# Kernel optimization log

Hardware: AMD Instinct MI355X
Metric: run time of the kernel (lower is better)

Reference implementation:

```python
import jax, jax.numpy as jnp
import numpy as np

NEG_SLOPE = 0.2


def add_self_loops(edge_index, num_nodes):
    loop = jnp.arange(num_nodes, dtype=edge_index.dtype)
    src = jnp.concatenate([edge_index[0], loop])
    dst = jnp.concatenate([edge_index[1], loop])
    return src, dst


def gat_conv(x, src, dst, W, att_src, att_dst, bias, heads, out_ch, concat):
    N = x.shape[0]
    h = (x @ W).reshape(N, heads, out_ch)                      # [N,H,C]
    a_src = jnp.sum(h * att_src, axis=-1)                      # [N,H]
    a_dst = jnp.sum(h * att_dst, axis=-1)                      # [N,H]
    e = a_src[src] + a_dst[dst]                                # [E,H]
    e = jax.nn.leaky_relu(e, NEG_SLOPE)
    # segment softmax over incoming edges of each destination node
    m = jax.ops.segment_max(e, dst, num_segments=N)            # [N,H]
    m = jnp.where(jnp.isfinite(m), m, 0.0)
    ex = jnp.exp(e - m[dst])
    s = jax.ops.segment_sum(ex, dst, num_segments=N)           # [N,H]
    alpha = ex / jnp.where(s[dst] > 0, s[dst], 1.0)            # [E,H]
    msg = alpha[:, :, None] * h[src]                           # [E,H,C]
    out = jax.ops.segment_sum(msg, dst, num_segments=N)        # [N,H,C]
    if concat:
        out = out.reshape(N, heads * out_ch)
    else:
        out = out.mean(axis=1)
    return out + bias


def setup_inputs() -> dict:
    key = jax.random.key(0)
    ks = jax.random.split(key, 10)
    N, F, E, H, C1 = 50000, 128, 800000, 8, 8
    x = jax.random.normal(ks[0], (N, F), dtype=jnp.float32)
    edge_index = jax.random.randint(ks[1], (2, E), 0, N, dtype=jnp.int64)
    sc = 0.1
    W1 = jax.random.normal(ks[2], (F, H * C1), dtype=jnp.float32) * sc
    a_src1 = jax.random.normal(ks[3], (H, C1), dtype=jnp.float32) * sc
    a_dst1 = jax.random.normal(ks[4], (H, C1), dtype=jnp.float32) * sc
    b1 = jnp.zeros((H * C1,), dtype=jnp.float32)
    W2 = jax.random.normal(ks[5], (H * C1, F), dtype=jnp.float32) * sc
    a_src2 = jax.random.normal(ks[6], (1, F), dtype=jnp.float32) * sc
    a_dst2 = jax.random.normal(ks[7], (1, F), dtype=jnp.float32) * sc
    b2 = jnp.zeros((F,), dtype=jnp.float32)
    return {"x": x, "edge_index": edge_index, "W1": W1, "a_src1": a_src1,
            "a_dst1": a_dst1, "b1": b1, "W2": W2, "a_src2": a_src2,
            "a_dst2": a_dst2, "b2": b2}


def reference(x, edge_index, W1, a_src1, a_dst1, b1, W2, a_src2, a_dst2, b2):
    N = x.shape[0]
    src, dst = add_self_loops(edge_index, N)
    h = gat_conv(x, src, dst, W1, a_src1, a_dst1, b1, heads=8, out_ch=8, concat=True)
    h = jax.nn.elu(h)
    out = gat_conv(h, src, dst, W2, a_src2, a_dst2, b2, heads=1, out_ch=x.shape[1], concat=True)
    return out
```

## Files before the change

### kernel.cpp

```cpp
#include <hip/hip_runtime.h>
#include <hip/hip_fp16.h>
#include <math.h>

#define NEG_SLOPE 0.2f
#define BSTRIDE 6144

typedef _Float16 f16x8 __attribute__((ext_vector_type(8)));
typedef float    f32x4 __attribute__((ext_vector_type(4)));

__device__ __forceinline__ void get_edge(const int* __restrict__ ei, int E, int e,
                                         int& s, int& d) {
    if (e < E) { s = ei[e]; d = ei[E + e]; }
    else       { s = e - E; d = e - E; }
}

union G1SMem {
    unsigned int sWu[4096];
    struct {
        int lhist[256], lbase[256], lrank[256], gbase[256];
        unsigned int sbuf[4096];
        int saddr[4096];
    } sc;
};

__global__ __launch_bounds__(256) void g1s_kernel(const float* __restrict__ x,
                                                  const float* __restrict__ W,
                                                  const float* __restrict__ asrc,
                                                  const float* __restrict__ adst,
                                                  _Float16* __restrict__ hout,
                                                  float* __restrict__ av,
                                                  float* __restrict__ bv, int N,
                                                  int gblocks,
                                                  const float* __restrict__ W2,
                                                  const float* __restrict__ as2,
                                                  const float* __restrict__ ad2,
                                                  float* __restrict__ wa,
                                                  float* __restrict__ wb,
                                                  int* __restrict__ bcur,
                                                  const int* __restrict__ ei, int E, int ET,
                                                  unsigned int* __restrict__ bstore,
                                                  int nbuck) {
    __shared__ G1SMem sm;
    int t = threadIdx.x;

    if (blockIdx.x == (unsigned)gblocks) {
        if (t < 64) {
            const float* wr = W2 + t * 128;
            float sa = 0.f, sb = 0.f;
#pragma unroll 8
            for (int c = 0; c < 128; ++c) {
                float w = wr[c];
                sa = fmaf(w, as2[c], sa);
                sb = fmaf(w, ad2[c], sb);
            }
            wa[t] = sa; wb[t] = sb;
        }
        return;
    }

    if (blockIdx.x > (unsigned)gblocks) {
        int sblk = blockIdx.x - gblocks - 1;
        int start = sblk * 4096;
        int cnt = ET - start; if (cnt > 4096) cnt = 4096;
        sm.sc.lhist[t] = 0; sm.sc.lrank[t] = 0;
        __syncthreads();
        int mybuck[16]; unsigned int myval[16];
#pragma unroll
        for (int k = 0; k < 16; ++k) {
            int e = start + t + k * 256;
            mybuck[k] = -1;
            if (e < ET) {
                int s, d; get_edge(ei, E, e, s, d);
                mybuck[k] = d >> 8;
                myval[k] = ((unsigned int)d << 16) | (unsigned int)s;
                atomicAdd(&sm.sc.lhist[mybuck[k]], 1);
            }
        }
        __syncthreads();
        int v = sm.sc.lhist[t];
        sm.sc.lbase[t] = v;
        __syncthreads();
        for (int off = 1; off < 256; off <<= 1) {
            int u = (t >= off) ? sm.sc.lbase[t - off] : 0;
            __syncthreads();
            sm.sc.lbase[t] += u;
            __syncthreads();
        }
        int excl = sm.sc.lbase[t] - v;
        if (t < nbuck && v > 0)
            sm.sc.gbase[t] = t * BSTRIDE + atomicAdd(&bcur[t], v);
        __syncthreads();
        sm.sc.lbase[t] = excl;
        __syncthreads();
#pragma unroll
        for (int k = 0; k < 16; ++k) {
            int b = mybuck[k];
            if (b >= 0) {
                int r = atomicAdd(&sm.sc.lrank[b], 1);
                int idx = sm.sc.lbase[b] + r;
                sm.sc.sbuf[idx] = myval[k];
                sm.sc.saddr[idx] = sm.sc.gbase[b] + r;
            }
        }
        __syncthreads();
        for (int j = t; j < cnt; j += 256)
            bstore[sm.sc.saddr[j]] = sm.sc.sbuf[j];
        return;
    }

    for (int p = t; p < 4096; p += 256) {
        int frag = p >> 8;
        int lane = (p >> 2) & 63;
        int j2   = p & 3;
        int chunk = frag >> 2, nt = frag & 3;
        int k = chunk * 32 + ((lane >> 4) << 3) + (j2 << 1);
        int n = nt * 16 + (lane & 15);
        union { _Float16 h[2]; unsigned int u; } pk;
        pk.h[0] = (_Float16)W[k * 64 + n];
        pk.h[1] = (_Float16)W[(k + 1) * 64 + n];
        sm.sWu[p] = pk.u;
    }
    __syncthreads();

    int lane = t & 63;
    int wid  = t >> 6;
    int rbase = blockIdx.x * 64 + wid * 16;
    int l15 = lane & 15, quad = lane >> 4;
    int rA = rbase + l15; if (rA >= N) rA = N - 1;

    const unsigned int* fragbase = &sm.sWu[lane * 4];
    f32x4 z = {0.f, 0.f, 0.f, 0.f};
    f32x4 acc[4] = {z, z, z, z};

#pragma unroll
    for (int chunk = 0; chunk < 4; ++chunk) {
        const float* xp = x + (size_t)rA * 128 + chunk * 32 + quad * 8;
        float4 f0 = *((const float4*)xp);
        float4 f1 = *((const float4*)(xp + 4));
        f16x8 af;
        af[0] = (_Float16)f0.x; af[1] = (_Float16)f0.y;
        af[2] = (_Float16)f0.z; af[3] = (_Float16)f0.w;
        af[4] = (_Float16)f1.x; af[5] = (_Float16)f1.y;
        af[6] = (_Float16)f1.z; af[7] = (_Float16)f1.w;
#pragma unroll
        for (int tt = 0; tt < 4; ++tt) {
            f16x8 bf = *((const f16x8*)(fragbase + (chunk * 4 + tt) * 256));
            acc[tt] = __builtin_amdgcn_mfma_f32_16x16x32_f16(af, bf, acc[tt], 0, 0, 0);
        }
    }

    float asc[4], adc[4];
#pragma unroll
    for (int tt = 0; tt < 4; ++tt) { asc[tt] = asrc[tt * 16 + l15]; adc[tt] = adst[tt * 16 + l15]; }
#pragma unroll
    for (int reg = 0; reg < 4; ++reg) {
        int r = rbase + quad * 4 + reg;
        bool ok = (r < N);
#pragma unroll
        for (int tt = 0; tt < 4; ++tt) {
            float v = acc[tt][reg];
            if (ok) hout[(size_t)r * 64 + tt * 16 + l15] = (_Float16)v;
            float pa = v * asc[tt], pb = v * adc[tt];
            pa += __shfl_xor(pa, 1); pb += __shfl_xor(pb, 1);
            pa += __shfl_xor(pa, 2); pb += __shfl_xor(pb, 2);
            pa += __shfl_xor(pa, 4); pb += __shfl_xor(pb, 4);
            if (ok && (lane & 7) == 0) {
                int head = tt * 2 + (l15 >> 3);
                av[r * 8 + head] = pa;
                bv[r * 8 + head] = pb;
            }
        }
    }
}

__global__ __launch_bounds__(256) void bucket_csr64(const unsigned int* __restrict__ bstore,
                                                    const int* __restrict__ bcur,
                                                    int* __restrict__ cnt,
                                                    unsigned short* __restrict__ col, int N) {
    __shared__ int lrank[256];
    int b = blockIdx.x, t = threadIdx.x;
    int base = b * BSTRIDE;
    int nb = bcur[b];
    lrank[t] = 0;
    __syncthreads();
    for (int i = t; i < nb; i += 256) {
        unsigned int pk = bstore[base + i];
        int local = (pk >> 16) & 255;
        int r = atomicAdd(&lrank[local], 1);
        if (r < 64) col[(((b << 8) + local) << 6) + r] = (unsigned short)(pk & 0xFFFFu);
    }
    __syncthreads();
    int node = (b << 8) + t;
    if (node < N) cnt[node] = lrank[t];
}

__global__ __launch_bounds__(512) void agg1_kernel(const int* __restrict__ cnt,
                                                   const unsigned short* __restrict__ col,
                                                   const float* __restrict__ av,
                                                   const float* __restrict__ bv,
                                                   const __half* __restrict__ h1,
                                                   const float* __restrict__ b1,
                                                   const float* __restrict__ wa,
                                                   const float* __restrict__ wb,
                                                   _Float16* __restrict__ out1,
                                                   float* __restrict__ av2,
                                                   float* __restrict__ bv2, int N) {
    int lane = threadIdx.x & 63;
    int node = blockIdx.x * 16 + (threadIdx.x >> 6) * 2 + (lane >> 5);
    bool valid = node < N;
    int nodeC = valid ? node : N - 1;
    int g  = (lane >> 3) & 3;
    int gl = lane & 7;
    int beg = nodeC << 6;
    int deg = cnt[nodeC]; if (deg > 64) deg = 64;
    int end = beg + deg;
    int last = end - 1;
    float bd = bv[nodeC * 8 + gl];
    const uint4* hrow = (const uint4*)h1;

    uint4 z4 = {0u, 0u, 0u, 0u};
    int e = beg + g;
    int c0 = col[e      <= last ? e      : last];
    int c1 = col[e + 4  <= last ? e + 4  : last];
    int c2 = col[e + 8  <= last ? e + 8  : last];
    float av0 = 0.f, av1v = 0.f; uint4 h0 = z4, h1v = z4;
    if (e < end)     { av0  = av[c0 * 8 + gl]; h0  = hrow[(size_t)c0 * 8 + gl]; }
    if (e + 4 < end) { av1v = av[c1 * 8 + gl]; h1v = hrow[(size_t)c1 * 8 + gl]; }

    float s = 0.f, a0 = 0.f, a1 = 0.f, a2 = 0.f, a3 = 0.f,
          a4 = 0.f, a5 = 0.f, a6 = 0.f, a7 = 0.f;
    for (; e < end; e += 4) {
        float av2v = 0.f; uint4 h2 = z4;
        if (e + 8 < end) { av2v = av[c2 * 8 + gl]; h2 = hrow[(size_t)c2 * 8 + gl]; }
        int c3 = col[e + 12 <= last ? e + 12 : last];
        float l = av0 + bd;
        l = l > 0.f ? l : NEG_SLOPE * l;
        float w = __expf(l);
        float2 f0 = __half22float2(*(const __half2*)&h0.x);
        float2 f1 = __half22float2(*(const __half2*)&h0.y);
        float2 f2 = __half22float2(*(const __half2*)&h0.z);
        float2 f3 = __half22float2(*(const __half2*)&h0.w);
        s += w;
        a0 = fmaf(w, f0.x, a0); a1 = fmaf(w, f0.y, a1);
        a2 = fmaf(w, f1.x, a2); a3 = fmaf(w, f1.y, a3);
        a4 = fmaf(w, f2.x, a4); a5 = fmaf(w, f2.y, a5);
        a6 = fmaf(w, f3.x, a6); a7 = fmaf(w, f3.y, a7);
        av0 = av1v; h0 = h1v; av1v = av2v; h1v = h2; c2 = c3;
    }
#pragma unroll
    for (int off = 8; off < 32; off <<= 1) {
        s  += __shfl_xor(s, off);
        a0 += __shfl_xor(a0, off); a1 += __shfl_xor(a1, off);
        a2 += __shfl_xor(a2, off); a3 += __shfl_xor(a3, off);
        a4 += __shfl_xor(a4, off); a5 += __shfl_xor(a5, off);
        a6 += __shfl_xor(a6, off); a7 += __shfl_xor(a7, off);
    }
    float inv = __builtin_amdgcn_rcpf(s);
    float4 bb0 = ((const float4*)b1)[gl * 2];
    float4 bb1 = ((const float4*)b1)[gl * 2 + 1];
    float v0 = a0 * inv + bb0.x, v1 = a1 * inv + bb0.y;
    float v2 = a2 * inv + bb0.z, v3 = a3 * inv + bb0.w;
    float v4 = a4 * inv + bb1.x, v5 = a5 * inv + bb1.y;
    float v6 = a6 * inv + bb1.z, v7 = a7 * inv + bb1.w;
    v0 = v0 > 0.f ? v0 : __expf(v0) - 1.f; v1 = v1 > 0.f ? v1 : __expf(v1) - 1.f;
    v2 = v2 > 0.f ? v2 : __expf(v2) - 1.f; v3 = v3 > 0.f ? v3 : __expf(v3) - 1.f;
    v4 = v4 > 0.f ? v4 : __expf(v4) - 1.f; v5 = v5 > 0.f ? v5 : __expf(v5) - 1.f;
    v6 = v6 > 0.f ? v6 : __expf(v6) - 1.f; v7 = v7 > 0.f ? v7 : __expf(v7) - 1.f;
    float4 wa0 = ((const float4*)wa)[gl * 2], wa1 = ((const float4*)wa)[gl * 2 + 1];
    float4 wb0 = ((const float4*)wb)[gl * 2], wb1 = ((const float4*)wb)[gl * 2 + 1];
    float pa = v0 * wa0.x + v1 * wa0.y + v2 * wa0.z + v3 * wa0.w
             + v4 * wa1.x + v5 * wa1.y + v6 * wa1.z + v7 * wa1.w;
    float pb = v0 * wb0.x + v1 * wb0.y + v2 * wb0.z + v3 * wb0.w
             + v4 * wb1.x + v5 * wb1.y + v6 * wb1.z + v7 * wb1.w;
    pa += __shfl_xor(pa, 1); pb += __shfl_xor(pb, 1);
    pa += __shfl_xor(pa, 2); pb += __shfl_xor(pb, 2);
    pa += __shfl_xor(pa, 4); pb += __shfl_xor(pb, 4);
    if (valid && (lane & 31) == 0) { av2[node] = pa; bv2[node] = pb; }
    if (valid && g == 0) {
        f16x8 o;
        o[0] = (_Float16)v0; o[1] = (_Float16)v1; o[2] = (_Float16)v2; o[3] = (_Float16)v3;
        o[4] = (_Float16)v4; o[5] = (_Float16)v5; o[6] = (_Float16)v6; o[7] = (_Float16)v7;
        ((f16x8*)out1)[(size_t)node * 8 + gl] = o;
    }
}

__global__ __launch_bounds__(512) void agg2g2_kernel(const int* __restrict__ cnt,
                                                     const unsigned short* __restrict__ col,
                                                     const float* __restrict__ av,
                                                     const float* __restrict__ bv,
                                                     const __half* __restrict__ out1,
                                                     const float* __restrict__ W,
                                                     const float* __restrict__ b2,
                                                     float* __restrict__ dout, int N) {
    __shared__ unsigned int sWu[4096];
    __shared__ _Float16 sAgg[64][72];
    int t = threadIdx.x;
    int lane = t & 63;
    int wid  = t >> 6;
    int rbase = blockIdx.x * 64;

    for (int p = t; p < 4096; p += 512) {
        int frag = p >> 8;
        int ln = (p >> 2) & 63;
        int j2 = p & 3;
        int chunk = frag >> 3, nt = frag & 7;
        int k = chunk * 32 + ((ln >> 4) << 3) + (j2 << 1);
        int n = nt * 16 + (ln & 15);
        union { _Float16 h[2]; unsigned int u; } pk;
        pk.h[0] = (_Float16)W[k * 128 + n];
        pk.h[1] = (_Float16)W[(k + 1) * 128 + n];
        sWu[p] = pk.u;
    }

    int g  = (lane >> 3) & 3;
    int gl = lane & 7;
    const uint4* hrow = (const uint4*)out1;
    uint4 z4 = {0u, 0u, 0u, 0u};
#pragma unroll 1
    for (int pass = 0; pass < 4; ++pass) {
        int nl = pass * 16 + wid * 2 + (lane >> 5);
        int node = rbase + nl;
        bool valid = node < N;
        int nodeC = valid ? node : N - 1;
        int beg = nodeC << 6;
        int deg = cnt[nodeC]; if (deg > 64) deg = 64;
        int end = beg + deg;
        int last = end - 1;
        float bd = bv[nodeC];

        int e = beg + g;
        int c0 = col[e      <= last ? e      : last];
        int c1 = col[e + 4  <= last ? e + 4  : last];
        int c2 = col[e + 8  <= last ? e + 8  : last];
        float av0 = 0.f, av1v = 0.f; uint4 h0 = z4, h1v = z4;
        if (e < end)     { av0  = av[c0]; h0  = hrow[(size_t)c0 * 8 + gl]; }
        if (e + 4 < end) { av1v = av[c1]; h1v = hrow[(size_t)c1 * 8 + gl]; }

        float s = 0.f, a0 = 0.f, a1 = 0.f, a2 = 0.f, a3 = 0.f,
              a4 = 0.f, a5 = 0.f, a6 = 0.f, a7 = 0.f;
        for (; e < end; e += 4) {
            float av2v = 0.f; uint4 h2 = z4;
            if (e + 8 < end) { av2v = av[c2]; h2 = hrow[(size_t)c2 * 8 + gl]; }
            int c3 = col[e + 12 <= last ? e + 12 : last];
            float l = av0 + bd;
            l = l > 0.f ? l : NEG_SLOPE * l;
            float w = __expf(l);
            float2 f0 = __half22float2(*(const __half2*)&h0.x);
            float2 f1 = __half22float2(*(const __half2*)&h0.y);
            float2 f2 = __half22float2(*(const __half2*)&h0.z);
            float2 f3 = __half22float2(*(const __half2*)&h0.w);
            s += w;
            a0 = fmaf(w, f0.x, a0); a1 = fmaf(w, f0.y, a1);
            a2 = fmaf(w, f1.x, a2); a3 = fmaf(w, f1.y, a3);
            a4 = fmaf(w, f2.x, a4); a5 = fmaf(w, f2.y, a5);
            a6 = fmaf(w, f3.x, a6); a7 = fmaf(w, f3.y, a7);
            av0 = av1v; h0 = h1v; av1v = av2v; h1v = h2; c2 = c3;
        }
#pragma unroll
        for (int off = 8; off < 32; off <<= 1) {
            s  += __shfl_xor(s, off);
            a0 += __shfl_xor(a0, off); a1 += __shfl_xor(a1, off);
            a2 += __shfl_xor(a2, off); a3 += __shfl_xor(a3, off);
            a4 += __shfl_xor(a4, off); a5 += __shfl_xor(a5, off);
            a6 += __shfl_xor(a6, off); a7 += __shfl_xor(a7, off);
        }
        if (g == 0) {
            float inv = __builtin_amdgcn_rcpf(s);
            f16x8 o;
            o[0] = (_Float16)(a0 * inv); o[1] = (_Float16)(a1 * inv);
            o[2] = (_Float16)(a2 * inv); o[3] = (_Float16)(a3 * inv);
            o[4] = (_Float16)(a4 * inv); o[5] = (_Float16)(a5 * inv);
            o[6] = (_Float16)(a6 * inv); o[7] = (_Float16)(a7 * inv);
            *((f16x8*)&sAgg[nl][gl * 8]) = o;
        }
    }
    __syncthreads();

    int rblk = (wid & 3) * 16;
    int chalf = wid >> 2;
    int l15 = lane & 15, quad = lane >> 4;

    const unsigned int* fragbase = &sWu[lane * 4];
    f32x4 z = {0.f, 0.f, 0.f, 0.f};
    f32x4 acc[4] = {z, z, z, z};

#pragma unroll
    for (int chunk = 0; chunk < 2; ++chunk) {
        f16x8 af = *((const f16x8*)&sAgg[rblk + l15][chunk * 32 + quad * 8]);
#pragma unroll
        for (int tt = 0; tt < 4; ++tt) {
            f16x8 bf = *((const f16x8*)(fragbase + (chunk * 8 + chalf * 4 + tt) * 256));
            acc[tt] = __builtin_amdgcn_mfma_f32_16x16x32_f16(af, bf, acc[tt], 0, 0, 0);
        }
    }

    float bcol[4];
#pragma unroll
    for (int tt = 0; tt < 4; ++tt) bcol[tt] = b2[chalf * 64 + tt * 16 + l15];
#pragma unroll
    for (int reg = 0; reg < 4; ++reg) {
        int r = rbase + rblk + quad * 4 + reg;
        if (r < N) {
#pragma unroll
            for (int tt = 0; tt < 4; ++tt)
                dout[(size_t)r * 128 + chalf * 64 + tt * 16 + l15] = acc[tt][reg] + bcol[tt];
        }
    }
}

extern "C" void kernel_launch(void* const* d_in, const int* in_sizes, int n_in,
                              void* d_out, int out_size, void* d_ws, size_t ws_size,
                              hipStream_t stream) {
    const float* x      = (const float*)d_in[0];
    const int*   ei     = (const int*)  d_in[1];
    const float* W1     = (const float*)d_in[2];
    const float* a_src1 = (const float*)d_in[3];
    const float* a_dst1 = (const float*)d_in[4];
    const float* b1     = (const float*)d_in[5];
    const float* W2     = (const float*)d_in[6];
    const float* a_src2 = (const float*)d_in[7];
    const float* a_dst2 = (const float*)d_in[8];
    const float* b2     = (const float*)d_in[9];
    float* dout = (float*)d_out;

    const int N  = in_sizes[0] / 128;
    const int E  = in_sizes[1] / 2;
    const int ET = E + N;
    const int NBUCK = (N + 255) >> 8;
    const int NBLKA = (ET + 4095) >> 12;

    char* wsb = (char*)d_ws;
    _Float16* h1     = (_Float16*)wsb; wsb += (size_t)N * 64 * 2;
    _Float16* out1   = (_Float16*)wsb; wsb += (size_t)N * 64 * 2;
    float* av1  = (float*)wsb; wsb += (size_t)N * 8 * 4;
    float* bv1  = (float*)wsb; wsb += (size_t)N * 8 * 4;
    float* av2  = (float*)wsb; wsb += (size_t)N * 4;
    float* bv2  = (float*)wsb; wsb += (size_t)N * 4;
    float* wa   = (float*)wsb; wsb += 64 * 4;
    float* wb   = (float*)wsb; wsb += 64 * 4;
    int* cnt    = (int*)wsb; wsb += (size_t)N * 4;
    unsigned short* col = (unsigned short*)wsb; wsb += (size_t)N * 64 * 2;
    unsigned int* bstore = (unsigned int*)wsb; wsb += (size_t)NBUCK * BSTRIDE * 4;
    int* bcur   = (int*)wsb; wsb += 256 * 4;

    const int B = 256;
    const int gblocks = (N + 63) / 64;

    hipMemsetAsync(bcur, 0, 256 * sizeof(int), stream);

    g1s_kernel<<<gblocks + 1 + NBLKA, B, 0, stream>>>(x, W1, a_src1, a_dst1, h1, av1, bv1, N,
                                                      gblocks, W2, a_src2, a_dst2, wa, wb,
                                                      bcur, ei, E, ET, bstore, NBUCK);

    bucket_csr64<<<NBUCK, B, 0, stream>>>(bstore, bcur, cnt, col, N);

    agg1_kernel<<<(N + 15) / 16, 512, 0, stream>>>(cnt, col, av1, bv1,
                                                   (const __half*)h1, b1, wa, wb,
                                                   out1, av2, bv2, N);

    agg2g2_kernel<<<gblocks, 512, 0, stream>>>(cnt, col, av2, bv2,
                                               (const __half*)out1, W2, b2, dout, N);
}
```

Measured before the change: 175.0 us.

## Replace global bucket CSR build with per-block sorted chunks ranked in aggregation kernels

The scatter kernel now writes each 4096-edge chunk locally sorted by destination bucket, plus per-chunk bucket offsets, instead of atomically appending into global buckets. The separate bucket_csr64 kernel and the memset go away. Each aggregation block instead scans every chunk's slice for its 256-node bucket and builds a 64-node column list in shared memory. This removes one launch, the global atomics and the col/cnt arrays. The cost is that every aggregation block, in both layers, walks all ~208 chunks and four blocks re-filter the same bucket data.

```diff
diff --git a/kernel.cpp b/kernel.cpp
--- a/kernel.cpp
+++ b/kernel.cpp
@@ -3,7 +3,6 @@
 #include <math.h>
 
 #define NEG_SLOPE 0.2f
-#define BSTRIDE 6144
 
 typedef _Float16 f16x8 __attribute__((ext_vector_type(8)));
 typedef float    f32x4 __attribute__((ext_vector_type(4)));
@@ -17,9 +16,8 @@
 union G1SMem {
     unsigned int sWu[4096];
     struct {
-        int lhist[256], lbase[256], lrank[256], gbase[256];
+        int lhist[256], lbase[256], lrank[256];
         unsigned int sbuf[4096];
-        int saddr[4096];
     } sc;
 };
 
@@ -36,10 +34,9 @@
                                                   const float* __restrict__ ad2,
                                                   float* __restrict__ wa,
                                                   float* __restrict__ wb,
-                                                  int* __restrict__ bcur,
                                                   const int* __restrict__ ei, int E, int ET,
                                                   unsigned int* __restrict__ bstore,
-                                                  int nbuck) {
+                                                  int* __restrict__ bofs) {
     __shared__ G1SMem sm;
     int t = threadIdx.x;
 
@@ -72,7 +69,7 @@
             if (e < ET) {
                 int s, d; get_edge(ei, E, e, s, d);
                 mybuck[k] = d >> 8;
-                myval[k] = ((unsigned int)d << 16) | (unsigned int)s;
+                myval[k] = ((unsigned int)(d & 255) << 16) | (unsigned int)s;
                 atomicAdd(&sm.sc.lhist[mybuck[k]], 1);
             }
         }
@@ -87,9 +84,7 @@
             __syncthreads();
         }
         int excl = sm.sc.lbase[t] - v;
-        if (t < nbuck && v > 0)
-            sm.sc.gbase[t] = t * BSTRIDE + atomicAdd(&bcur[t], v);
-        __syncthreads();
+        bofs[(sblk << 8) + t] = excl;
         sm.sc.lbase[t] = excl;
         __syncthreads();
 #pragma unroll
@@ -97,14 +92,12 @@
             int b = mybuck[k];
             if (b >= 0) {
                 int r = atomicAdd(&sm.sc.lrank[b], 1);
-                int idx = sm.sc.lbase[b] + r;
-                sm.sc.sbuf[idx] = myval[k];
-                sm.sc.saddr[idx] = sm.sc.gbase[b] + r;
+                sm.sc.sbuf[sm.sc.lbase[b] + r] = myval[k];
             }
         }
         __syncthreads();
         for (int j = t; j < cnt; j += 256)
-            bstore[sm.sc.saddr[j]] = sm.sc.sbuf[j];
+            bstore[start + j] = sm.sc.sbuf[j];
         return;
     }
 
@@ -173,29 +166,34 @@
     }
 }
 
-__global__ __launch_bounds__(256) void bucket_csr64(const unsigned int* __restrict__ bstore,
-                                                    const int* __restrict__ bcur,
-                                                    int* __restrict__ cnt,
-                                                    unsigned short* __restrict__ col, int N) {
-    __shared__ int lrank[256];
-    int b = blockIdx.x, t = threadIdx.x;
-    int base = b * BSTRIDE;
-    int nb = bcur[b];
-    lrank[t] = 0;
+__device__ __forceinline__ void rank_quarter(const unsigned int* __restrict__ bstore,
+                                             const int* __restrict__ bofs,
+                                             int b, int q, int ET, int nblk,
+                                             unsigned short (*colL)[64],
+                                             int* lrank) {
+    int t = threadIdx.x;
+    if (t < 64) lrank[t] = 0;
     __syncthreads();
-    for (int i = t; i < nb; i += 256) {
-        unsigned int pk = bstore[base + i];
-        int local = (pk >> 16) & 255;
-        int r = atomicAdd(&lrank[local], 1);
-        if (r < 64) col[(((b << 8) + local) << 6) + r] = (unsigned short)(pk & 0xFFFFu);
+    int lane = t & 63, wid = t >> 6;
+    for (int sblk = wid; sblk < nblk; sblk += 8) {
+        int base = sblk << 12;
+        int cnt = ET - base; if (cnt > 4096) cnt = 4096;
+        int beg = bofs[(sblk << 8) + b];
+        int end = (b < 255) ? bofs[(sblk << 8) + b + 1] : cnt;
+        for (int i = beg + lane; i < end; i += 64) {
+            unsigned int pk = bstore[base + i];
+            int local = pk >> 16;
+            if ((local >> 6) == q) {
+                int r = atomicAdd(&lrank[local & 63], 1);
+                if (r < 64) colL[local & 63][r] = (unsigned short)(pk & 0xFFFFu);
+            }
+        }
     }
     __syncthreads();
-    int node = (b << 8) + t;
-    if (node < N) cnt[node] = lrank[t];
-}
-
-__global__ __launch_bounds__(512) void agg1_kernel(const int* __restrict__ cnt,
-                                                   const unsigned short* __restrict__ col,
+}
+
+__global__ __launch_bounds__(512) void agg1_kernel(const unsigned int* __restrict__ bstore,
+                                                   const int* __restrict__ bofs,
                                                    const float* __restrict__ av,
                                                    const float* __restrict__ bv,
                                                    const __half* __restrict__ h1,
@@ -204,144 +202,44 @@
                                                    const float* __restrict__ wb,
                                                    _Float16* __restrict__ out1,
                                                    float* __restrict__ av2,
-                                                   float* __restrict__ bv2, int N) {
+                                                   float* __restrict__ bv2,
+                                                   int N, int ET, int nblk) {
+    __shared__ unsigned short colL[64][64];
+    __shared__ int lrank[64];
+    int blk = blockIdx.x;
+    rank_quarter(bstore, bofs, blk >> 2, blk & 3, ET, nblk, colL, lrank);
+
     int lane = threadIdx.x & 63;
-    int node = blockIdx.x * 16 + (threadIdx.x >> 6) * 2 + (lane >> 5);
-    bool valid = node < N;
-    int nodeC = valid ? node : N - 1;
+    int wid  = threadIdx.x >> 6;
     int g  = (lane >> 3) & 3;
     int gl = lane & 7;
-    int beg = nodeC << 6;
-    int deg = cnt[nodeC]; if (deg > 64) deg = 64;
-    int end = beg + deg;
-    int last = end - 1;
-    float bd = bv[nodeC * 8 + gl];
     const uint4* hrow = (const uint4*)h1;
-
     uint4 z4 = {0u, 0u, 0u, 0u};
-    int e = beg + g;
-    int c0 = col[e      <= last ? e      : last];
-    int c1 = col[e + 4  <= last ? e + 4  : last];
-    int c2 = col[e + 8  <= last ? e + 8  : last];
-    float av0 = 0.f, av1v = 0.f; uint4 h0 = z4, h1v = z4;
-    if (e < end)     { av0  = av[c0 * 8 + gl]; h0  = hrow[(size_t)c0 * 8 + gl]; }
-    if (e + 4 < end) { av1v = av[c1 * 8 + gl]; h1v = hrow[(size_t)c1 * 8 + gl]; }
-
-    float s = 0.f, a0 = 0.f, a1 = 0.f, a2 = 0.f, a3 = 0.f,
-          a4 = 0.f, a5 = 0.f, a6 = 0.f, a7 = 0.f;
-    for (; e < end; e += 4) {
-        float av2v = 0.f; uint4 h2 = z4;
-        if (e + 8 < end) { av2v = av[c2 * 8 + gl]; h2 = hrow[(size_t)c2 * 8 + gl]; }
-        int c3 = col[e + 12 <= last ? e + 12 : last];
-        float l = av0 + bd;
-        l = l > 0.f ? l : NEG_SLOPE * l;
-        float w = __expf(l);
-        float2 f0 = __half22float2(*(const __half2*)&h0.x);
-        float2 f1 = __half22float2(*(const __half2*)&h0.y);
-        float2 f2 = __half22float2(*(const __half2*)&h0.z);
-        float2 f3 = __half22float2(*(const __half2*)&h0.w);
-        s += w;
-        a0 = fmaf(w, f0.x, a0); a1 = fmaf(w, f0.y, a1);
-        a2 = fmaf(w, f1.x, a2); a3 = fmaf(w, f1.y, a3);
-        a4 = fmaf(w, f2.x, a4); a5 = fmaf(w, f2.y, a5);
-        a6 = fmaf(w, f3.x, a6); a7 = fmaf(w, f3.y, a7);
-        av0 = av1v; h0 = h1v; av1v = av2v; h1v = h2; c2 = c3;
-    }
-#pragma unroll
-    for (int off = 8; off < 32; off <<= 1) {
-        s  += __shfl_xor(s, off);
-        a0 += __shfl_xor(a0, off); a1 += __shfl_xor(a1, off);
-        a2 += __shfl_xor(a2, off); a3 += __shfl_xor(a3, off);
-        a4 += __shfl_xor(a4, off); a5 += __shfl_xor(a5, off);
-        a6 += __shfl_xor(a6, off); a7 += __shfl_xor(a7, off);
-    }
-    float inv = __builtin_amdgcn_rcpf(s);
-    float4 bb0 = ((const float4*)b1)[gl * 2];
-    float4 bb1 = ((const float4*)b1)[gl * 2 + 1];
-    float v0 = a0 * inv + bb0.x, v1 = a1 * inv + bb0.y;
-    float v2 = a2 * inv + bb0.z, v3 = a3 * inv + bb0.w;
-    float v4 = a4 * inv + bb1.x, v5 = a5 * inv + bb1.y;
-    float v6 = a6 * inv + bb1.z, v7 = a7 * inv + bb1.w;
-    v0 = v0 > 0.f ? v0 : __expf(v0) - 1.f; v1 = v1 > 0.f ? v1 : __expf(v1) - 1.f;
-    v2 = v2 > 0.f ? v2 : __expf(v2) - 1.f; v3 = v3 > 0.f ? v3 : __expf(v3) - 1.f;
-    v4 = v4 > 0.f ? v4 : __expf(v4) - 1.f; v5 = v5 > 0.f ? v5 : __expf(v5) - 1.f;
-    v6 = v6 > 0.f ? v6 : __expf(v6) - 1.f; v7 = v7 > 0.f ? v7 : __expf(v7) - 1.f;
-    float4 wa0 = ((const float4*)wa)[gl * 2], wa1 = ((const float4*)wa)[gl * 2 + 1];
-    float4 wb0 = ((const float4*)wb)[gl * 2], wb1 = ((const float4*)wb)[gl * 2 + 1];
-    float pa = v0 * wa0.x + v1 * wa0.y + v2 * wa0.z + v3 * wa0.w
-             + v4 * wa1.x + v5 * wa1.y + v6 * wa1.z + v7 * wa1.w;
-    float pb = v0 * wb0.x + v1 * wb0.y + v2 * wb0.z + v3 * wb0.w
-             + v4 * wb1.x + v5 * wb1.y + v6 * wb1.z + v7 * wb1.w;
-    pa += __shfl_xor(pa, 1); pb += __shfl_xor(pb, 1);
-    pa += __shfl_xor(pa, 2); pb += __shfl_xor(pb, 2);
-    pa += __shfl_xor(pa, 4); pb += __shfl_xor(pb, 4);
-    if (valid && (lane & 31) == 0) { av2[node] = pa; bv2[node] = pb; }
-    if (valid && g == 0) {
-        f16x8 o;
-        o[0] = (_Float16)v0; o[1] = (_Float16)v1; o[2] = (_Float16)v2; o[3] = (_Float16)v3;
-        o[4] = (_Float16)v4; o[5] = (_Float16)v5; o[6] = (_Float16)v6; o[7] = (_Float16)v7;
-        ((f16x8*)out1)[(size_t)node * 8 + gl] = o;
-    }
-}
-
-__global__ __launch_bounds__(512) void agg2g2_kernel(const int* __restrict__ cnt,
-                                                     const unsigned short* __restrict__ col,
-                                                     const float* __restrict__ av,
-                                                     const float* __restrict__ bv,
-                                                     const __half* __restrict__ out1,
-                                                     const float* __restrict__ W,
-                                                     const float* __restrict__ b2,
-                                                     float* __restrict__ dout, int N) {
-    __shared__ unsigned int sWu[4096];
-    __shared__ _Float16 sAgg[64][72];
-    int t = threadIdx.x;
-    int lane = t & 63;
-    int wid  = t >> 6;
-    int rbase = blockIdx.x * 64;
-
-    for (int p = t; p < 4096; p += 512) {
-        int frag = p >> 8;
-        int ln = (p >> 2) & 63;
-        int j2 = p & 3;
-        int chunk = frag >> 3, nt = frag & 7;
-        int k = chunk * 32 + ((ln >> 4) << 3) + (j2 << 1);
-        int n = nt * 16 + (ln & 15);
-        union { _Float16 h[2]; unsigned int u; } pk;
-        pk.h[0] = (_Float16)W[k * 128 + n];
-        pk.h[1] = (_Float16)W[(k + 1) * 128 + n];
-        sWu[p] = pk.u;
-    }
-
-    int g  = (lane >> 3) & 3;
-    int gl = lane & 7;
-    const uint4* hrow = (const uint4*)out1;
-    uint4 z4 = {0u, 0u, 0u, 0u};
+
 #pragma unroll 1
     for (int pass = 0; pass < 4; ++pass) {
         int nl = pass * 16 + wid * 2 + (lane >> 5);
-        int node = rbase + nl;
+        int node = blk * 64 + nl;
         bool valid = node < N;
-        int nodeC = valid ? node : N - 1;
-        int beg = nodeC << 6;
-        int deg = cnt[nodeC]; if (deg > 64) deg = 64;
-        int end = beg + deg;
-        int last = end - 1;
-        float bd = bv[nodeC];
-
-        int e = beg + g;
-        int c0 = col[e      <= last ? e      : last];
-        int c1 = col[e + 4  <= last ? e + 4  : last];
-        int c2 = col[e + 8  <= last ? e + 8  : last];
+        int nodeC = valid ? node : 0;
+        int deg = lrank[nl]; if (deg > 64) deg = 64;
+        int last = deg - 1; if (last < 0) last = 0;
+        float bd = bv[nodeC * 8 + gl];
+
+        int e = g;
+        int c0 = colL[nl][e      <= last ? e      : last];
+        int c1 = colL[nl][e + 4  <= last ? e + 4  : last];
+        int c2 = colL[nl][e + 8  <= last ? e + 8  : last];
         float av0 = 0.f, av1v = 0.f; uint4 h0 = z4, h1v = z4;
-        if (e < end)     { av0  = av[c0]; h0  = hrow[(size_t)c0 * 8 + gl]; }
-        if (e + 4 < end) { av1v = av[c1]; h1v = hrow[(size_t)c1 * 8 + gl]; }
+        if (e < deg)     { av0  = av[c0 * 8 + gl]; h0  = hrow[(size_t)c0 * 8 + gl]; }
+        if (e + 4 < deg) { av1v = av[c1 * 8 + gl]; h1v = hrow[(size_t)c1 * 8 + gl]; }
 
         float s = 0.f, a0 = 0.f, a1 = 0.f, a2 = 0.f, a3 = 0.f,
               a4 = 0.f, a5 = 0.f, a6 = 0.f, a7 = 0.f;
-        for (; e < end; e += 4) {
+        for (; e < deg; e += 4) {
             float av2v = 0.f; uint4 h2 = z4;
-            if (e + 8 < end) { av2v = av[c2]; h2 = hrow[(size_t)c2 * 8 + gl]; }
-            int c3 = col[e + 12 <= last ? e + 12 : last];
+            if (e + 8 < deg) { av2v = av[c2 * 8 + gl]; h2 = hrow[(size_t)c2 * 8 + gl]; }
+            int c3 = colL[nl][e + 12 <= last ? e + 12 : last];
             float l = av0 + bd;
             l = l > 0.f ? l : NEG_SLOPE * l;
             float w = __expf(l);
@@ -364,8 +262,112 @@
             a4 += __shfl_xor(a4, off); a5 += __shfl_xor(a5, off);
             a6 += __shfl_xor(a6, off); a7 += __shfl_xor(a7, off);
         }
+        float inv = s > 0.f ? __builtin_amdgcn_rcpf(s) : 0.f;
+        float4 bb0 = ((const float4*)b1)[gl * 2];
+        float4 bb1 = ((const float4*)b1)[gl * 2 + 1];
+        float v0 = a0 * inv + bb0.x, v1 = a1 * inv + bb0.y;
+        float v2 = a2 * inv + bb0.z, v3 = a3 * inv + bb0.w;
+        float v4 = a4 * inv + bb1.x, v5 = a5 * inv + bb1.y;
+        float v6 = a6 * inv + bb1.z, v7 = a7 * inv + bb1.w;
+        v0 = v0 > 0.f ? v0 : __expf(v0) - 1.f; v1 = v1 > 0.f ? v1 : __expf(v1) - 1.f;
+        v2 = v2 > 0.f ? v2 : __expf(v2) - 1.f; v3 = v3 > 0.f ? v3 : __expf(v3) - 1.f;
+        v4 = v4 > 0.f ? v4 : __expf(v4) - 1.f; v5 = v5 > 0.f ? v5 : __expf(v5) - 1.f;
+        v6 = v6 > 0.f ? v6 : __expf(v6) - 1.f; v7 = v7 > 0.f ? v7 : __expf(v7) - 1.f;
+        float4 wa0 = ((const float4*)wa)[gl * 2], wa1 = ((const float4*)wa)[gl * 2 + 1];
+        float4 wb0 = ((const float4*)wb)[gl * 2], wb1 = ((const float4*)wb)[gl * 2 + 1];
+        float pa = v0 * wa0.x + v1 * wa0.y + v2 * wa0.z + v3 * wa0.w
+                 + v4 * wa1.x + v5 * wa1.y + v6 * wa1.z + v7 * wa1.w;
+        float pb = v0 * wb0.x + v1 * wb0.y + v2 * wb0.z + v3 * wb0.w
+                 + v4 * wb1.x + v5 * wb1.y + v6 * wb1.z + v7 * wb1.w;
+        pa += __shfl_xor(pa, 1); pb += __shfl_xor(pb, 1);
+        pa += __shfl_xor(pa, 2); pb += __shfl_xor(pb, 2);
+        pa += __shfl_xor(pa, 4); pb += __shfl_xor(pb, 4);
+        if (valid && (lane & 31) == 0) { av2[node] = pa; bv2[node] = pb; }
+        if (valid && g == 0) {
+            f16x8 o;
+            o[0] = (_Float16)v0; o[1] = (_Float16)v1; o[2] = (_Float16)v2; o[3] = (_Float16)v3;
+            o[4] = (_Float16)v4; o[5] = (_Float16)v5; o[6] = (_Float16)v6; o[7] = (_Float16)v7;
+            ((f16x8*)out1)[(size_t)node * 8 + gl] = o;
+        }
+    }
+}
+
+union A2Mem {
+    struct { unsigned short colL[64][64]; int lrank[64]; } rk;
+    unsigned int sWu[4096];
+};
+
+__global__ __launch_bounds__(512) void agg2g2_kernel(const unsigned int* __restrict__ bstore,
+                                                     const int* __restrict__ bofs,
+                                                     const float* __restrict__ av,
+                                                     const float* __restrict__ bv,
+                                                     const __half* __restrict__ out1,
+                                                     const float* __restrict__ W,
+                                                     const float* __restrict__ b2,
+                                                     float* __restrict__ dout,
+                                                     int N, int ET, int nblk) {
+    __shared__ A2Mem sm;
+    __shared__ _Float16 sAgg[64][72];
+    int blk = blockIdx.x;
+    int t = threadIdx.x;
+    int lane = t & 63;
+    int wid  = t >> 6;
+    int rbase = blk * 64;
+
+    rank_quarter(bstore, bofs, blk >> 2, blk & 3, ET, nblk, sm.rk.colL, sm.rk.lrank);
+
+    int g  = (lane >> 3) & 3;
+    int gl = lane & 7;
+    const uint4* hrow = (const uint4*)out1;
+    uint4 z4 = {0u, 0u, 0u, 0u};
+#pragma unroll 1
+    for (int pass = 0; pass < 4; ++pass) {
+        int nl = pass * 16 + wid * 2 + (lane >> 5);
+        int node = rbase + nl;
+        bool valid = node < N;
+        int nodeC = valid ? node : 0;
+        int deg = sm.rk.lrank[nl]; if (deg > 64) deg = 64;
+        int last = deg - 1; if (last < 0) last = 0;
+        float bd = bv[nodeC];
+
+        int e = g;
+        int c0 = sm.rk.colL[nl][e      <= last ? e      : last];
+        int c1 = sm.rk.colL[nl][e + 4  <= last ? e + 4  : last];
+        int c2 = sm.rk.colL[nl][e + 8  <= last ? e + 8  : last];
+        float av0 = 0.f, av1v = 0.f; uint4 h0 = z4, h1v = z4;
+        if (e < deg)     { av0  = av[c0]; h0  = hrow[(size_t)c0 * 8 + gl]; }
+        if (e + 4 < deg) { av1v = av[c1]; h1v = hrow[(size_t)c1 * 8 + gl]; }
+
+        float s = 0.f, a0 = 0.f, a1 = 0.f, a2 = 0.f, a3 = 0.f,
+              a4 = 0.f, a5 = 0.f, a6 = 0.f, a7 = 0.f;
+        for (; e < deg; e += 4) {
+            float av2v = 0.f; uint4 h2 = z4;
+            if (e + 8 < deg) { av2v = av[c2]; h2 = hrow[(size_t)c2 * 8 + gl]; }
+            int c3 = sm.rk.colL[nl][e + 12 <= last ? e + 12 : last];
+            float l = av0 + bd;
+            l = l > 0.f ? l : NEG_SLOPE * l;
+            float w = __expf(l);
+            float2 f0 = __half22float2(*(const __half2*)&h0.x);
+            float2 f1 = __half22float2(*(const __half2*)&h0.y);
+            float2 f2 = __half22float2(*(const __half2*)&h0.z);
+            float2 f3 = __half22float2(*(const __half2*)&h0.w);
+            s += w;
+            a0 = fmaf(w, f0.x, a0); a1 = fmaf(w, f0.y, a1);
+            a2 = fmaf(w, f1.x, a2); a3 = fmaf(w, f1.y, a3);
+            a4 = fmaf(w, f2.x, a4); a5 = fmaf(w, f2.y, a5);
+            a6 = fmaf(w, f3.x, a6); a7 = fmaf(w, f3.y, a7);
+            av0 = av1v; h0 = h1v; av1v = av2v; h1v = h2; c2 = c3;
+        }
+#pragma unroll
+        for (int off = 8; off < 32; off <<= 1) {
+            s  += __shfl_xor(s, off);
+            a0 += __shfl_xor(a0, off); a1 += __shfl_xor(a1, off);
+            a2 += __shfl_xor(a2, off); a3 += __shfl_xor(a3, off);
+            a4 += __shfl_xor(a4, off); a5 += __shfl_xor(a5, off);
+            a6 += __shfl_xor(a6, off); a7 += __shfl_xor(a7, off);
+        }
         if (g == 0) {
-            float inv = __builtin_amdgcn_rcpf(s);
+            float inv = s > 0.f ? __builtin_amdgcn_rcpf(s) : 0.f;
             f16x8 o;
             o[0] = (_Float16)(a0 * inv); o[1] = (_Float16)(a1 * inv);
             o[2] = (_Float16)(a2 * inv); o[3] = (_Float16)(a3 * inv);
@@ -376,11 +378,25 @@
     }
     __syncthreads();
 
+    for (int p = t; p < 4096; p += 512) {
+        int frag = p >> 8;
+        int ln = (p >> 2) & 63;
+        int j2 = p & 3;
+        int chunk = frag >> 3, nt = frag & 7;
+        int k = chunk * 32 + ((ln >> 4) << 3) + (j2 << 1);
+        int n = nt * 16 + (ln & 15);
+        union { _Float16 h[2]; unsigned int u; } pk;
+        pk.h[0] = (_Float16)W[k * 128 + n];
+        pk.h[1] = (_Float16)W[(k + 1) * 128 + n];
+        sm.sWu[p] = pk.u;
+    }
+    __syncthreads();
+
     int rblk = (wid & 3) * 16;
     int chalf = wid >> 2;
     int l15 = lane & 15, quad = lane >> 4;
 
-    const unsigned int* fragbase = &sWu[lane * 4];
+    const unsigned int* fragbase = &sm.sWu[lane * 4];
     f32x4 z = {0.f, 0.f, 0.f, 0.f};
     f32x4 acc[4] = {z, z, z, z};
 
@@ -426,8 +442,8 @@
     const int N  = in_sizes[0] / 128;
     const int E  = in_sizes[1] / 2;
     const int ET = E + N;
-    const int NBUCK = (N + 255) >> 8;
     const int NBLKA = (ET + 4095) >> 12;
+    const int NB64  = (N + 63) >> 6;
 
     char* wsb = (char*)d_ws;
     _Float16* h1     = (_Float16*)wsb; wsb += (size_t)N * 64 * 2;
@@ -438,26 +454,20 @@
     float* bv2  = (float*)wsb; wsb += (size_t)N * 4;
     float* wa   = (float*)wsb; wsb += 64 * 4;
     float* wb   = (float*)wsb; wsb += 64 * 4;
-    int* cnt    = (int*)wsb; wsb += (size_t)N * 4;
-    unsigned short* col = (unsigned short*)wsb; wsb += (size_t)N * 64 * 2;
-    unsigned int* bstore = (unsigned int*)wsb; wsb += (size_t)NBUCK * BSTRIDE * 4;
-    int* bcur   = (int*)wsb; wsb += 256 * 4;
-
-    const int B = 256;
+    unsigned int* bstore = (unsigned int*)wsb; wsb += (size_t)NBLKA * 4096 * 4;
+    int* bofs   = (int*)wsb; wsb += (size_t)NBLKA * 256 * 4;
+
     const int gblocks = (N + 63) / 64;
 
-    hipMemsetAsync(bcur, 0, 256 * sizeof(int), stream);
-
-    g1s_kernel<<<gblocks + 1 + NBLKA, B, 0, stream>>>(x, W1, a_src1, a_dst1, h1, av1, bv1, N,
-                                                      gblocks, W2, a_src2, a_dst2, wa, wb,
-                                                      bcur, ei, E, ET, bstore, NBUCK);
-
-    bucket_csr64<<<NBUCK, B, 0, stream>>>(bstore, bcur, cnt, col, N);
-
-    agg1_kernel<<<(N + 15) / 16, 512, 0, stream>>>(cnt, col, av1, bv1,
-                                                   (const __half*)h1, b1, wa, wb,
-                                                   out1, av2, bv2, N);
-
-    agg2g2_kernel<<<gblocks, 512, 0, stream>>>(cnt, col, av2, bv2,
-                                               (const __half*)out1, W2, b2, dout, N);
-}
+    g1s_kernel<<<gblocks + 1 + NBLKA, 256, 0, stream>>>(x, W1, a_src1, a_dst1, h1, av1, bv1, N,
+                                                        gblocks, W2, a_src2, a_dst2, wa, wb,
+                                                        ei, E, ET, bstore, bofs);
+
+    agg1_kernel<<<NB64, 512, 0, stream>>>(bstore, bofs, av1, bv1,
+                                          (const __half*)h1, b1, wa, wb,
+                                          out1, av2, bv2, N, ET, NBLKA);
+
+    agg2g2_kernel<<<NB64, 512, 0, stream>>>(bstore, bofs, av2, bv2,
+                                            (const __half*)out1, W2, b2, dout,
+                                            N, ET, NBLKA);
+}
```

Result: slower. 211.6 us (+20.9%).

## Pad CSR neighbor lists with sentinel node and use exp2 with prescaled logits

Applied to the files above, without the earlier changes.

Neighbor lists are padded to a multiple of four with a dummy node index N, whose attention logit is a large negative value and whose feature row is zero. This lets both aggregation loops drop per-edge bounds clamps and conditional loads. Attention vectors are also prescaled by log2(e) so the kernels can use the native exp2 instruction instead of __expf. The cost is a few extra padded iterations per node and extra workspace rows, plus a guard for a zero softmax sum.

```diff
diff --git a/kernel.cpp b/kernel.cpp
--- a/kernel.cpp
+++ b/kernel.cpp
@@ -4,6 +4,7 @@
 
 #define NEG_SLOPE 0.2f
 #define BSTRIDE 6144
+#define L2E 1.4426950408889634f
 
 typedef _Float16 f16x8 __attribute__((ext_vector_type(8)));
 typedef float    f32x4 __attribute__((ext_vector_type(4)));
@@ -39,7 +40,9 @@
                                                   int* __restrict__ bcur,
                                                   const int* __restrict__ ei, int E, int ET,
                                                   unsigned int* __restrict__ bstore,
-                                                  int nbuck) {
+                                                  int nbuck,
+                                                  float* __restrict__ av2,
+                                                  _Float16* __restrict__ out1p) {
     __shared__ G1SMem sm;
     int t = threadIdx.x;
 
@@ -53,8 +56,12 @@
                 sa = fmaf(w, as2[c], sa);
                 sb = fmaf(w, ad2[c], sb);
             }
-            wa[t] = sa; wb[t] = sb;
-        }
+            wa[t] = sa * L2E; wb[t] = sb * L2E;
+        }
+        if (t < 8)  av[(size_t)N * 8 + t] = -1.0e5f;
+        if (t == 8) av2[N] = -1.0e5f;
+        if (t >= 64 && t < 128)  hout[(size_t)N * 64 + (t - 64)]  = (_Float16)0.f;
+        if (t >= 128 && t < 192) out1p[(size_t)N * 64 + (t - 128)] = (_Float16)0.f;
         return;
     }
 
@@ -151,7 +158,10 @@
 
     float asc[4], adc[4];
 #pragma unroll
-    for (int tt = 0; tt < 4; ++tt) { asc[tt] = asrc[tt * 16 + l15]; adc[tt] = adst[tt * 16 + l15]; }
+    for (int tt = 0; tt < 4; ++tt) {
+        asc[tt] = asrc[tt * 16 + l15] * L2E;
+        adc[tt] = adst[tt * 16 + l15] * L2E;
+    }
 #pragma unroll
     for (int reg = 0; reg < 4; ++reg) {
         int r = rbase + quad * 4 + reg;
@@ -191,7 +201,15 @@
     }
     __syncthreads();
     int node = (b << 8) + t;
-    if (node < N) cnt[node] = lrank[t];
+    if (node < N) {
+        int deg = lrank[t]; if (deg > 64) deg = 64;
+        int degP = (deg + 3) & ~3; if (degP > 64) degP = 64;
+        cnt[node] = degP;
+        int padEnd = degP + 12; if (padEnd > 64) padEnd = 64;
+        unsigned short ph = (unsigned short)N;
+        size_t rb = (size_t)node << 6;
+        for (int i = deg; i < padEnd; ++i) col[rb + i] = ph;
+    }
 }
 
 __global__ __launch_bounds__(512) void agg1_kernel(const int* __restrict__ cnt,
@@ -208,34 +226,30 @@
     int lane = threadIdx.x & 63;
     int node = blockIdx.x * 16 + (threadIdx.x >> 6) * 2 + (lane >> 5);
     bool valid = node < N;
-    int nodeC = valid ? node : N - 1;
+    int nodeC = valid ? node : 0;
     int g  = (lane >> 3) & 3;
     int gl = lane & 7;
-    int beg = nodeC << 6;
-    int deg = cnt[nodeC]; if (deg > 64) deg = 64;
-    int end = beg + deg;
-    int last = end - 1;
+    const unsigned short* colp = col + ((size_t)nodeC << 6);
+    int degP = cnt[nodeC];
     float bd = bv[nodeC * 8 + gl];
     const uint4* hrow = (const uint4*)h1;
 
-    uint4 z4 = {0u, 0u, 0u, 0u};
-    int e = beg + g;
-    int c0 = col[e      <= last ? e      : last];
-    int c1 = col[e + 4  <= last ? e + 4  : last];
-    int c2 = col[e + 8  <= last ? e + 8  : last];
-    float av0 = 0.f, av1v = 0.f; uint4 h0 = z4, h1v = z4;
-    if (e < end)     { av0  = av[c0 * 8 + gl]; h0  = hrow[(size_t)c0 * 8 + gl]; }
-    if (e + 4 < end) { av1v = av[c1 * 8 + gl]; h1v = hrow[(size_t)c1 * 8 + gl]; }
+    int e = g;
+    int c0 = colp[e];
+    int c1 = colp[e + 4];
+    int c2 = colp[e + 8];
+    float av0  = av[c0 * 8 + gl]; uint4 h0  = hrow[(size_t)c0 * 8 + gl];
+    float av1v = av[c1 * 8 + gl]; uint4 h1v = hrow[(size_t)c1 * 8 + gl];
 
     float s = 0.f, a0 = 0.f, a1 = 0.f, a2 = 0.f, a3 = 0.f,
           a4 = 0.f, a5 = 0.f, a6 = 0.f, a7 = 0.f;
-    for (; e < end; e += 4) {
-        float av2v = 0.f; uint4 h2 = z4;
-        if (e + 8 < end) { av2v = av[c2 * 8 + gl]; h2 = hrow[(size_t)c2 * 8 + gl]; }
-        int c3 = col[e + 12 <= last ? e + 12 : last];
+    for (; e < degP; e += 4) {
+        float av2v = av[c2 * 8 + gl];
+        uint4 h2   = hrow[(size_t)c2 * 8 + gl];
+        int c3 = colp[e + 12];
         float l = av0 + bd;
         l = l > 0.f ? l : NEG_SLOPE * l;
-        float w = __expf(l);
+        float w = __builtin_amdgcn_exp2f(l);
         float2 f0 = __half22float2(*(const __half2*)&h0.x);
         float2 f1 = __half22float2(*(const __half2*)&h0.y);
         float2 f2 = __half22float2(*(const __half2*)&h0.z);
@@ -255,7 +269,7 @@
         a4 += __shfl_xor(a4, off); a5 += __shfl_xor(a5, off);
         a6 += __shfl_xor(a6, off); a7 += __shfl_xor(a7, off);
     }
-    float inv = __builtin_amdgcn_rcpf(s);
+    float inv = s > 0.f ? __builtin_amdgcn_rcpf(s) : 0.f;
     float4 bb0 = ((const float4*)b1)[gl * 2];
     float4 bb1 = ((const float4*)b1)[gl * 2 + 1];
     float v0 = a0 * inv + bb0.x, v1 = a1 * inv + bb0.y;
@@ -315,36 +329,32 @@
     int g  = (lane >> 3) & 3;
     int gl = lane & 7;
     const uint4* hrow = (const uint4*)out1;
-    uint4 z4 = {0u, 0u, 0u, 0u};
 #pragma unroll 1
     for (int pass = 0; pass < 4; ++pass) {
         int nl = pass * 16 + wid * 2 + (lane >> 5);
         int node = rbase + nl;
         bool valid = node < N;
-        int nodeC = valid ? node : N - 1;
-        int beg = nodeC << 6;
-        int deg = cnt[nodeC]; if (deg > 64) deg = 64;
-        int end = beg + deg;
-        int last = end - 1;
+        int nodeC = valid ? node : 0;
+        const unsigned short* colp = col + ((size_t)nodeC << 6);
+        int degP = cnt[nodeC];
         float bd = bv[nodeC];
 
-        int e = beg + g;
-        int c0 = col[e      <= last ? e      : last];
-        int c1 = col[e + 4  <= last ? e + 4  : last];
-        int c2 = col[e + 8  <= last ? e + 8  : last];
-        float av0 = 0.f, av1v = 0.f; uint4 h0 = z4, h1v = z4;
-        if (e < end)     { av0  = av[c0]; h0  = hrow[(size_t)c0 * 8 + gl]; }
-        if (e + 4 < end) { av1v = av[c1]; h1v = hrow[(size_t)c1 * 8 + gl]; }
+        int e = g;
+        int c0 = colp[e];
+        int c1 = colp[e + 4];
+        int c2 = colp[e + 8];
+        float av0  = av[c0]; uint4 h0  = hrow[(size_t)c0 * 8 + gl];
+        float av1v = av[c1]; uint4 h1v = hrow[(size_t)c1 * 8 + gl];
 
         float s = 0.f, a0 = 0.f, a1 = 0.f, a2 = 0.f, a3 = 0.f,
               a4 = 0.f, a5 = 0.f, a6 = 0.f, a7 = 0.f;
-        for (; e < end; e += 4) {
-            float av2v = 0.f; uint4 h2 = z4;
-            if (e + 8 < end) { av2v = av[c2]; h2 = hrow[(size_t)c2 * 8 + gl]; }
-            int c3 = col[e + 12 <= last ? e + 12 : last];
+        for (; e < degP; e += 4) {
+            float av2v = av[c2];
+            uint4 h2   = hrow[(size_t)c2 * 8 + gl];
+            int c3 = colp[e + 12];
             float l = av0 + bd;
             l = l > 0.f ? l : NEG_SLOPE * l;
-            float w = __expf(l);
+            float w = __builtin_amdgcn_exp2f(l);
             float2 f0 = __half22float2(*(const __half2*)&h0.x);
             float2 f1 = __half22float2(*(const __half2*)&h0.y);
             float2 f2 = __half22float2(*(const __half2*)&h0.z);
@@ -365,7 +375,7 @@
             a6 += __shfl_xor(a6, off); a7 += __shfl_xor(a7, off);
         }
         if (g == 0) {
-            float inv = __builtin_amdgcn_rcpf(s);
+            float inv = s > 0.f ? __builtin_amdgcn_rcpf(s) : 0.f;
             f16x8 o;
             o[0] = (_Float16)(a0 * inv); o[1] = (_Float16)(a1 * inv);
             o[2] = (_Float16)(a2 * inv); o[3] = (_Float16)(a3 * inv);
@@ -430,29 +440,29 @@
     const int NBLKA = (ET + 4095) >> 12;
 
     char* wsb = (char*)d_ws;
-    _Float16* h1     = (_Float16*)wsb; wsb += (size_t)N * 64 * 2;
-    _Float16* out1   = (_Float16*)wsb; wsb += (size_t)N * 64 * 2;
-    float* av1  = (float*)wsb; wsb += (size_t)N * 8 * 4;
+    _Float16* h1     = (_Float16*)wsb; wsb += (size_t)(N + 1) * 64 * 2;
+    _Float16* out1   = (_Float16*)wsb; wsb += (size_t)(N + 1) * 64 * 2;
+    float* av1  = (float*)wsb; wsb += (size_t)(N + 1) * 8 * 4;
     float* bv1  = (float*)wsb; wsb += (size_t)N * 8 * 4;
-    float* av2  = (float*)wsb; wsb += (size_t)N * 4;
+    float* av2  = (float*)wsb; wsb += (size_t)(N + 1) * 4;
     float* bv2  = (float*)wsb; wsb += (size_t)N * 4;
     float* wa   = (float*)wsb; wsb += 64 * 4;
     float* wb   = (float*)wsb; wsb += 64 * 4;
     int* cnt    = (int*)wsb; wsb += (size_t)N * 4;
-    unsigned short* col = (unsigned short*)wsb; wsb += (size_t)N * 64 * 2;
+    unsigned short* col = (unsigned short*)wsb; wsb += ((size_t)N * 64 + 64) * 2;
     unsigned int* bstore = (unsigned int*)wsb; wsb += (size_t)NBUCK * BSTRIDE * 4;
     int* bcur   = (int*)wsb; wsb += 256 * 4;
 
-    const int B = 256;
     const int gblocks = (N + 63) / 64;
 
     hipMemsetAsync(bcur, 0, 256 * sizeof(int), stream);
 
-    g1s_kernel<<<gblocks + 1 + NBLKA, B, 0, stream>>>(x, W1, a_src1, a_dst1, h1, av1, bv1, N,
-                                                      gblocks, W2, a_src2, a_dst2, wa, wb,
-                                                      bcur, ei, E, ET, bstore, NBUCK);
-
-    bucket_csr64<<<NBUCK, B, 0, stream>>>(bstore, bcur, cnt, col, N);
+    g1s_kernel<<<gblocks + 1 + NBLKA, 256, 0, stream>>>(x, W1, a_src1, a_dst1, h1, av1, bv1, N,
+                                                        gblocks, W2, a_src2, a_dst2, wa, wb,
+                                                        bcur, ei, E, ET, bstore, NBUCK,
+                                                        av2, out1);
+
+    bucket_csr64<<<NBUCK, 256, 0, stream>>>(bstore, bcur, cnt, col, N);
 
     agg1_kernel<<<(N + 15) / 16, 512, 0, stream>>>(cnt, col, av1, bv1,
                                                    (const __half*)h1, b1, wa, wb,
```

Result: slower. 182.3 us (+4.2%).
